# Optimization experiments

Measured on AMD Instinct MI355X. Metric: run time of the kernel, lower is better.

## Reference

```python
import jax, jax.numpy as jnp
import numpy as np

B = 2048
REAL_NL = 500
NL = 504            # ceil(500/8)*8
NZ = 50
NC = 21
GH = 512            # gru hidden
LRF = 336           # low_res_features
CHS = [336, 168, 84, 42]  # deconv channel ladder
EPS = 1e-5


def setup_inputs() -> dict:
    key = jax.random.key(0)
    ks = iter(jax.random.split(key, 40))
    d = {}
    d["X"] = jax.random.normal(next(ks), (B, REAL_NL, NC), dtype=jnp.float32)
    d["z"] = jax.random.normal(next(ks), (B, NZ), dtype=jnp.float32)
    d["is_training"] = 0
    # Upsampler dense: Linear(NZ -> NL//8 * LRF)
    d["dense_W"] = jax.random.normal(next(ks), (NL // 8 * LRF, NZ), dtype=jnp.float32) * 0.05
    d["dense_b"] = jnp.zeros((NL // 8 * LRF,), dtype=jnp.float32)
    for i in range(3):
        cin, cout = CHS[i], CHS[i + 1]
        d[f"dc{i}_W"] = jax.random.normal(next(ks), (cin, cout, 2), dtype=jnp.float32) * 0.05
        d[f"bn{i}_g"] = jnp.ones((cout,), dtype=jnp.float32)
        d[f"bn{i}_b"] = jnp.zeros((cout,), dtype=jnp.float32)
        d[f"bn{i}_m"] = jax.random.normal(next(ks), (cout,), dtype=jnp.float32) * 0.1
        d[f"bn{i}_v"] = jax.random.uniform(next(ks), (cout,), dtype=jnp.float32, minval=0.5, maxval=1.5)
        d[f"prelu{i}"] = jnp.full((1,), 0.25, dtype=jnp.float32)
    # project_x: Conv1d(NC->NC, k=1) == linear
    d["w_px"] = jax.random.normal(next(ks), (NC, NC), dtype=jnp.float32) * 0.05
    d["b_px"] = jnp.zeros((NC,), dtype=jnp.float32)
    # GRU (1 layer): input = 42 + NC = 63
    gin = CHS[3] + NC
    d["w_ih"] = jax.random.normal(next(ks), (3 * GH, gin), dtype=jnp.float32) * 0.05
    d["w_hh"] = jax.random.normal(next(ks), (3 * GH, GH), dtype=jnp.float32) * 0.05
    d["b_ih"] = jnp.zeros((3 * GH,), dtype=jnp.float32)
    d["b_hh"] = jnp.zeros((3 * GH,), dtype=jnp.float32)
    # output_x: Conv1d(GH->NC, k=1)
    d["w_out"] = jax.random.normal(next(ks), (NC, GH), dtype=jnp.float32) * 0.05
    d["b_out"] = jnp.zeros((NC,), dtype=jnp.float32)
    return d


def _upsample(z, dense_W, dense_b, dcs, bns, alphas):
    b = z.shape[0]
    h = (z @ dense_W.T + dense_b).reshape(b, LRF, NL // 8)  # [B, 336, 63]
    for i in range(3):
        W = dcs[i]  # [cin, cout, 2]
        t = h.shape[-1]
        # ConvTranspose1d k=2 s=2: out[..., 2t+k] = sum_c in[...,c,t] * W[c,:,k]
        h = jnp.einsum('bct,cok->botk', h, W).reshape(b, W.shape[1], 2 * t)
        g, bb, m, v = bns[i]
        h = (h - m[:, None]) * (g[:, None] / jnp.sqrt(v[:, None] + EPS)) + bb[:, None]
        a = alphas[i]
        h = jnp.where(h >= 0, h, a[0] * h)
    return h  # [B, 42, NL]


def reference(X, z, is_training,
              dense_W, dense_b,
              dc0_W, bn0_g, bn0_b, bn0_m, bn0_v, prelu0,
              dc1_W, bn1_g, bn1_b, bn1_m, bn1_v, prelu1,
              dc2_W, bn2_g, bn2_b, bn2_m, bn2_v, prelu2,
              w_px, b_px, w_ih, w_hh, b_ih, b_hh, w_out, b_out):
    h = _upsample(z, dense_W, dense_b,
                  [dc0_W, dc1_W, dc2_W],
                  [(bn0_g, bn0_b, bn0_m, bn0_v), (bn1_g, bn1_b, bn1_m, bn1_v), (bn2_g, bn2_b, bn2_m, bn2_v)],
                  [prelu0, prelu1, prelu2])
    b = z.shape[0]
    hseq = jnp.transpose(h, (2, 0, 1))  # [NL, B, 42]

    def step(carry, h_t):
        gru_h, x1h = carry                       # [B,GH], [B,NC]
        px = x1h @ w_px.T + b_px                 # project_x (1x1 conv)
        x_in = jnp.concatenate([h_t, px], axis=-1)  # [B, 63]
        gi = x_in @ w_ih.T + b_ih
        gh = gru_h @ w_hh.T + b_hh
        ir, iz, inn = jnp.split(gi, 3, axis=-1)
        hr, hz, hn = jnp.split(gh, 3, axis=-1)
        r = jax.nn.sigmoid(ir + hr)
        zt = jax.nn.sigmoid(iz + hz)
        n = jnp.tanh(inn + r * hn)
        h_new = (1.0 - zt) * n + zt * gru_h
        logit = h_new @ w_out.T + b_out          # [B, NC]
        x1h_new = jax.nn.one_hot(jnp.argmax(logit, axis=-1), NC, dtype=logit.dtype)
        return (h_new, x1h_new), logit

    init = (jnp.zeros((b, GH), dtype=z.dtype), jnp.zeros((b, NC), dtype=z.dtype))
    _, logits = jax.lax.scan(step, init, hseq)   # [NL, B, NC]
    out = jnp.transpose(logits, (1, 0, 2))[:, :REAL_NL, :]
    return out
```

## Files before the change

kernel.cpp:

```cpp
#include <hip/hip_runtime.h>
#include <math.h>

#define NLFULL 504
#define REAL_NL 500
#define BATCH 2048
#define NZ 50
#define NC 21
#define GHID 512
#define EPSB 1e-5f

typedef __attribute__((ext_vector_type(4))) float f32x4;
typedef __attribute__((ext_vector_type(8))) short short8;

__device__ __forceinline__ unsigned short f2bf(float x) {
    unsigned u = __builtin_bit_cast(unsigned, x);
    unsigned r = (u + 0x7FFFu + ((u >> 16) & 1u)) >> 16;
    return (unsigned short)r;
}
__device__ __forceinline__ float bf2f(unsigned short h) {
    unsigned u = ((unsigned)h) << 16;
    return __builtin_bit_cast(float, u);
}

__global__ __launch_bounds__(512) void upsample_kernel(
    const float* __restrict__ z, const float* __restrict__ dW, const float* __restrict__ db,
    const float* __restrict__ W0, const float* __restrict__ g0, const float* __restrict__ bb0,
    const float* __restrict__ m0, const float* __restrict__ v0, const float* __restrict__ al0,
    const float* __restrict__ W1, const float* __restrict__ g1, const float* __restrict__ bb1,
    const float* __restrict__ m1, const float* __restrict__ v1, const float* __restrict__ al1,
    const float* __restrict__ W2, const float* __restrict__ g2, const float* __restrict__ bb2,
    const float* __restrict__ m2, const float* __restrict__ v2, const float* __restrict__ al2,
    float* __restrict__ hseq)
{
    __shared__ float bufA[5712];
    __shared__ float bufB[5544];
    __shared__ float zl[52];

    const int b   = blockIdx.x;
    const int ta  = blockIdx.y * 16;
    const int nt0 = min(16, 63 - ta);
    const int tid = threadIdx.x;

    if (tid < NZ) zl[tid] = z[b * NZ + tid];
    __syncthreads();

    for (int i = tid; i < 336 * nt0; i += 512) {
        int c = i % 336, tt = i / 336;
        int row = c * 63 + ta + tt;
        const float* wr = dW + (size_t)row * NZ;
        float s = db[row];
        #pragma unroll
        for (int n = 0; n < NZ; ++n) s += zl[n] * wr[n];
        bufA[c * 17 + tt] = s;
    }
    __syncthreads();

    const float a0 = al0[0], a1 = al1[0], a2 = al2[0];

    for (int i = tid; i < 168 * 2 * nt0; i += 512) {
        int o = i % 168, tt1 = i / 168;
        int tt = tt1 >> 1, k = tt1 & 1;
        const float* wp = W0 + o * 2 + k;
        float s = 0.f;
        for (int c = 0; c < 336; ++c) s += bufA[c * 17 + tt] * wp[c * 336];
        float sc = g0[o] / sqrtf(v0[o] + EPSB);
        s = (s - m0[o]) * sc + bb0[o];
        s = (s >= 0.f) ? s : a0 * s;
        bufB[o * 33 + tt1] = s;
    }
    __syncthreads();

    for (int i = tid; i < 84 * 4 * nt0; i += 512) {
        int o = i % 84, tt2 = i / 84;
        int tt1 = tt2 >> 1, k = tt2 & 1;
        const float* wp = W1 + o * 2 + k;
        float s = 0.f;
        for (int c = 0; c < 168; ++c) s += bufB[c * 33 + tt1] * wp[c * 168];
        float sc = g1[o] / sqrtf(v1[o] + EPSB);
        s = (s - m1[o]) * sc + bb1[o];
        s = (s >= 0.f) ? s : a1 * s;
        bufA[o * 65 + tt2] = s;
    }
    __syncthreads();

    for (int i = tid; i < 42 * 8 * nt0; i += 512) {
        int o = i % 42, tt3 = i / 42;
        int tt2 = tt3 >> 1, k = tt3 & 1;
        const float* wp = W2 + o * 2 + k;
        float s = 0.f;
        for (int c = 0; c < 84; ++c) s += bufA[c * 65 + tt2] * wp[c * 84];
        float sc = g2[o] / sqrtf(v2[o] + EPSB);
        s = (s - m2[o]) * sc + bb2[o];
        s = (s >= 0.f) ? s : a2 * s;
        int t3 = 8 * ta + tt3;
        hseq[(size_t)t3 * (BATCH * 42) + b * 42 + o] = s;
    }
}

__global__ void table_kernel(const float* __restrict__ w_px, const float* __restrict__ b_px,
                             const float* __restrict__ w_ih, const float* __restrict__ b_ih,
                             float* __restrict__ table)
{
    int i = blockIdx.x * 256 + threadIdx.x;
    if (i >= 22 * 1536) return;
    int e = i / 1536, jg = i % 1536;
    const float* wih = w_ih + jg * 63 + 42;
    float s = b_ih[jg];
    #pragma unroll
    for (int jp = 0; jp < NC; ++jp) {
        float px = b_px[jp] + (e < NC ? w_px[jp * NC + e] : 0.f);
        s += px * wih[jp];
    }
    table[i] = s;
}

__global__ void pack_whh_kernel(const float* __restrict__ w_hh,
                                unsigned short* __restrict__ pH,
                                unsigned short* __restrict__ pM,
                                unsigned short* __restrict__ pL)
{
    int i = blockIdx.x * 256 + threadIdx.x;
    if (i >= 3 * 32 * 16 * 512) return;
    int e = i & 7, l = (i >> 3) & 63, kf = (i >> 9) & 15, nf = (i >> 13) & 31, g = i >> 18;
    int n = nf * 16 + (l & 15);
    int k = kf * 32 + ((l >> 4) << 3) + e;
    float v = w_hh[(size_t)(g * GHID + n) * GHID + k];
    unsigned short h1 = f2bf(v);       float r1 = v - bf2f(h1);
    unsigned short h2 = f2bf(r1);      float r2 = r1 - bf2f(h2);
    unsigned short h3 = f2bf(r2);
    pH[i] = h1; pM[i] = h2; pL[i] = h3;
}

__global__ void pack_wih_kernel(const float* __restrict__ w_ih,
                                unsigned short* __restrict__ pH,
                                unsigned short* __restrict__ pM,
                                unsigned short* __restrict__ pL)
{
    int i = blockIdx.x * 256 + threadIdx.x;
    if (i >= 3 * 32 * 2 * 512) return;
    int e = i & 7, l = (i >> 3) & 63, kf = (i >> 9) & 1, nf = (i >> 10) & 31, g = i >> 15;
    int n = nf * 16 + (l & 15);
    int k = kf * 32 + ((l >> 4) << 3) + e;
    float v = (k < 42) ? w_ih[(size_t)(g * GHID + n) * 63 + k] : 0.f;
    unsigned short h1 = f2bf(v);       float r1 = v - bf2f(h1);
    unsigned short h2 = f2bf(r1);      float r2 = r1 - bf2f(h2);
    unsigned short h3 = f2bf(r2);
    pH[i] = h1; pM[i] = h2; pL[i] = h3;
}

__global__ void init_kernel(unsigned short* __restrict__ hH, unsigned short* __restrict__ hM,
                            unsigned short* __restrict__ hL, int* __restrict__ idx)
{
    int i = blockIdx.x * 256 + threadIdx.x;
    if (i < BATCH * GHID) { hH[i] = 0; hM[i] = 0; hL[i] = 0; }
    if (i < BATCH) idx[i] = NC;
}

#define MFMA6(acc, aH_, aM_, aL_, bH_, bM_, bL_)                                  \
    acc = __builtin_amdgcn_mfma_f32_16x16x32_bf16(aH_, bH_, acc, 0, 0, 0);        \
    acc = __builtin_amdgcn_mfma_f32_16x16x32_bf16(aH_, bM_, acc, 0, 0, 0);        \
    acc = __builtin_amdgcn_mfma_f32_16x16x32_bf16(aM_, bH_, acc, 0, 0, 0);        \
    acc = __builtin_amdgcn_mfma_f32_16x16x32_bf16(aH_, bL_, acc, 0, 0, 0);        \
    acc = __builtin_amdgcn_mfma_f32_16x16x32_bf16(aL_, bH_, acc, 0, 0, 0);        \
    acc = __builtin_amdgcn_mfma_f32_16x16x32_bf16(aM_, bM_, acc, 0, 0, 0);

__global__ __launch_bounds__(128) void gru_gates_mfma(
    const unsigned short* __restrict__ hpH, const unsigned short* __restrict__ hpM,
    const unsigned short* __restrict__ hpL,
    const float* __restrict__ ht,
    const int* __restrict__ idx, const float* __restrict__ table,
    const unsigned short* __restrict__ whhH, const unsigned short* __restrict__ whhM,
    const unsigned short* __restrict__ whhL,
    const unsigned short* __restrict__ wihH, const unsigned short* __restrict__ wihM,
    const unsigned short* __restrict__ wihL,
    const float* __restrict__ b_hh,
    unsigned short* __restrict__ hnH, unsigned short* __restrict__ hnM,
    unsigned short* __restrict__ hnL)
{
    const int l  = threadIdx.x & 63;
    const int wv = threadIdx.x >> 6;
    const int m0 = blockIdx.x * 64 + wv * 32;
    const int nf0 = blockIdx.y * 2;
    const int lrow = l & 15;
    const int lk = (l >> 4) << 3;

    f32x4 accRZ[2][2][2];
    f32x4 accIN[2][2];
    f32x4 accHN[2][2];
    #pragma unroll
    for (int a = 0; a < 2; ++a)
        #pragma unroll
        for (int b = 0; b < 2; ++b) {
            accRZ[0][a][b] = (f32x4)0.f; accRZ[1][a][b] = (f32x4)0.f;
            accIN[a][b] = (f32x4)0.f;    accHN[a][b] = (f32x4)0.f;
        }

    const size_t arow0 = (size_t)(m0 + lrow) * GHID + lk;
    const size_t arow1 = arow0 + 16 * GHID;

    for (int kf = 0; kf < 16; ++kf) {
        short8 aH[2], aM[2], aL[2];
        aH[0] = *(const short8*)(hpH + arow0 + kf * 32);
        aM[0] = *(const short8*)(hpM + arow0 + kf * 32);
        aL[0] = *(const short8*)(hpL + arow0 + kf * 32);
        aH[1] = *(const short8*)(hpH + arow1 + kf * 32);
        aM[1] = *(const short8*)(hpM + arow1 + kf * 32);
        aL[1] = *(const short8*)(hpL + arow1 + kf * 32);
        #pragma unroll
        for (int g = 0; g < 3; ++g) {
            #pragma unroll
            for (int ni = 0; ni < 2; ++ni) {
                size_t boff = ((size_t)((g * 32 + nf0 + ni) * 16 + kf) << 9) + (l << 3);
                short8 bH = *(const short8*)(whhH + boff);
                short8 bM = *(const short8*)(whhM + boff);
                short8 bL = *(const short8*)(whhL + boff);
                #pragma unroll
                for (int mi = 0; mi < 2; ++mi) {
                    f32x4* acc = (g == 2) ? &accHN[mi][ni] : &accRZ[g][mi][ni];
                    MFMA6((*acc), aH[mi], aM[mi], aL[mi], bH, bM, bL);
                }
            }
        }
    }

    #pragma unroll
    for (int kf = 0; kf < 2; ++kf) {
        short8 aH[2], aM[2], aL[2];
        #pragma unroll
        for (int mi = 0; mi < 2; ++mi) {
            const float* rp = ht + (size_t)(m0 + mi * 16 + lrow) * 42;
            #pragma unroll
            for (int e = 0; e < 8; ++e) {
                int k = kf * 32 + lk + e;
                float f = (k < 42) ? rp[k] : 0.f;
                unsigned short h1 = f2bf(f);  float r1 = f - bf2f(h1);
                unsigned short h2 = f2bf(r1); float r2 = r1 - bf2f(h2);
                aH[mi][e] = (short)h1;
                aM[mi][e] = (short)h2;
                aL[mi][e] = (short)f2bf(r2);
            }
        }
        #pragma unroll
        for (int g = 0; g < 3; ++g) {
            #pragma unroll
            for (int ni = 0; ni < 2; ++ni) {
                size_t boff = ((size_t)((g * 32 + nf0 + ni) * 2 + kf) << 9) + (l << 3);
                short8 bH = *(const short8*)(wihH + boff);
                short8 bM = *(const short8*)(wihM + boff);
                short8 bL = *(const short8*)(wihL + boff);
                #pragma unroll
                for (int mi = 0; mi < 2; ++mi) {
                    f32x4* acc = (g == 2) ? &accIN[mi][ni] : &accRZ[g][mi][ni];
                    MFMA6((*acc), aH[mi], aM[mi], aL[mi], bH, bM, bL);
                }
            }
        }
    }

    #pragma unroll
    for (int ni = 0; ni < 2; ++ni) {
        int c = (nf0 + ni) * 16 + lrow;
        float bhr = b_hh[c], bhz = b_hh[GHID + c], bhn = b_hh[2 * GHID + c];
        #pragma unroll
        for (int mi = 0; mi < 2; ++mi) {
            #pragma unroll
            for (int r = 0; r < 4; ++r) {
                int m = m0 + mi * 16 + ((l >> 4) << 2) + r;
                const float* tb = table + idx[m] * 1536;
                float rv = accRZ[0][mi][ni][r] + bhr + tb[c];
                float zv = accRZ[1][mi][ni][r] + bhz + tb[GHID + c];
                float rg = 1.f / (1.f + expf(-rv));
                float zg = 1.f / (1.f + expf(-zv));
                float nv = accIN[mi][ni][r] + tb[2 * GHID + c] + rg * (accHN[mi][ni][r] + bhn);
                float ng = tanhf(nv);
                size_t off = (size_t)m * GHID + c;
                float hpv = bf2f(hpH[off]) + bf2f(hpM[off]) + bf2f(hpL[off]);
                float hnv = (1.f - zg) * ng + zg * hpv;
                unsigned short h1 = f2bf(hnv);  float r1 = hnv - bf2f(h1);
                unsigned short h2 = f2bf(r1);   float r2 = r1 - bf2f(h2);
                hnH[off] = h1;
                hnM[off] = h2;
                hnL[off] = f2bf(r2);
            }
        }
    }
}

__global__ __launch_bounds__(256) void gru_logits(
    const unsigned short* __restrict__ hH, const unsigned short* __restrict__ hM,
    const unsigned short* __restrict__ hL,
    const float* __restrict__ w_out, const float* __restrict__ b_out,
    float* __restrict__ out, int* __restrict__ idx, int t)
{
    const int wave = threadIdx.x >> 6, lane = threadIdx.x & 63;
    const int b = blockIdx.x * 4 + wave;

    const size_t base = (size_t)b * GHID + lane * 8;
    float hv[8];
    #pragma unroll
    for (int j = 0; j < 8; ++j)
        hv[j] = bf2f(hH[base + j]) + bf2f(hM[base + j]) + bf2f(hL[base + j]);

    float acc[NC];
    #pragma unroll
    for (int c = 0; c < NC; ++c) {
        const float* wr = w_out + c * GHID + lane * 8;
        float s = 0.f;
        #pragma unroll
        for (int j = 0; j < 8; ++j) s += hv[j] * wr[j];
        acc[c] = s;
    }
    #pragma unroll
    for (int off = 32; off > 0; off >>= 1) {
        #pragma unroll
        for (int c = 0; c < NC; ++c) acc[c] += __shfl_xor(acc[c], off);
    }
    float best = -1e30f; int bi = 0;
    #pragma unroll
    for (int c = 0; c < NC; ++c) {
        acc[c] += b_out[c];
        if (acc[c] > best) { best = acc[c]; bi = c; }
    }
    if (t < REAL_NL && lane < NC)
        out[(size_t)b * (REAL_NL * NC) + t * NC + lane] = acc[lane];
    if (lane == 0) idx[b] = bi;
}

extern "C" void kernel_launch(void* const* d_in, const int* in_sizes, int n_in,
                              void* d_out, int out_size, void* d_ws, size_t ws_size,
                              hipStream_t stream)
{
    const float* z    = (const float*)d_in[1];
    const float* dW   = (const float*)d_in[3];
    const float* db   = (const float*)d_in[4];
    const float* W0   = (const float*)d_in[5];
    const float* g0   = (const float*)d_in[6];
    const float* bb0  = (const float*)d_in[7];
    const float* m0   = (const float*)d_in[8];
    const float* v0   = (const float*)d_in[9];
    const float* al0  = (const float*)d_in[10];
    const float* W1   = (const float*)d_in[11];
    const float* g1   = (const float*)d_in[12];
    const float* bb1  = (const float*)d_in[13];
    const float* m1   = (const float*)d_in[14];
    const float* v1   = (const float*)d_in[15];
    const float* al1  = (const float*)d_in[16];
    const float* W2   = (const float*)d_in[17];
    const float* g2   = (const float*)d_in[18];
    const float* bb2  = (const float*)d_in[19];
    const float* m2   = (const float*)d_in[20];
    const float* v2   = (const float*)d_in[21];
    const float* al2  = (const float*)d_in[22];
    const float* w_px = (const float*)d_in[23];
    const float* b_px = (const float*)d_in[24];
    const float* w_ih = (const float*)d_in[25];
    const float* w_hh = (const float*)d_in[26];
    const float* b_ih = (const float*)d_in[27];
    const float* b_hh = (const float*)d_in[28];
    const float* w_out= (const float*)d_in[29];
    const float* b_out= (const float*)d_in[30];
    float* out = (float*)d_out;

    float* ws = (float*)d_ws;
    float* hseq = ws;
    unsigned short* hAH = (unsigned short*)(hseq + (size_t)NLFULL * BATCH * 42);
    unsigned short* hAM = hAH + (size_t)BATCH * GHID;
    unsigned short* hAL = hAM + (size_t)BATCH * GHID;
    unsigned short* hBH = hAL + (size_t)BATCH * GHID;
    unsigned short* hBM = hBH + (size_t)BATCH * GHID;
    unsigned short* hBL = hBM + (size_t)BATCH * GHID;
    unsigned short* whhH = hBL + (size_t)BATCH * GHID;
    unsigned short* whhM = whhH + 3 * 32 * 16 * 512;
    unsigned short* whhL = whhM + 3 * 32 * 16 * 512;
    unsigned short* wihH = whhL + 3 * 32 * 16 * 512;
    unsigned short* wihM = wihH + 3 * 32 * 2 * 512;
    unsigned short* wihL = wihM + 3 * 32 * 2 * 512;
    float* table = (float*)(wihL + 3 * 32 * 2 * 512);
    int*   idx   = (int*)(table + 22 * 1536);

    upsample_kernel<<<dim3(BATCH, 4), 512, 0, stream>>>(
        z, dW, db,
        W0, g0, bb0, m0, v0, al0,
        W1, g1, bb1, m1, v1, al1,
        W2, g2, bb2, m2, v2, al2,
        hseq);

    table_kernel<<<(22 * 1536 + 255) / 256, 256, 0, stream>>>(w_px, b_px, w_ih, b_ih, table);
    pack_whh_kernel<<<(3 * 32 * 16 * 512 + 255) / 256, 256, 0, stream>>>(w_hh, whhH, whhM, whhL);
    pack_wih_kernel<<<(3 * 32 * 2 * 512 + 255) / 256, 256, 0, stream>>>(w_ih, wihH, wihM, wihL);
    init_kernel<<<(BATCH * GHID + 255) / 256, 256, 0, stream>>>(hAH, hAM, hAL, idx);

    for (int t = 0; t < NLFULL; ++t) {
        const unsigned short* pH = (t & 1) ? hBH : hAH;
        const unsigned short* pM = (t & 1) ? hBM : hAM;
        const unsigned short* pL = (t & 1) ? hBL : hAL;
        unsigned short* nH = (t & 1) ? hAH : hBH;
        unsigned short* nM = (t & 1) ? hAM : hBM;
        unsigned short* nL = (t & 1) ? hAL : hBL;
        gru_gates_mfma<<<dim3(32, 16), 128, 0, stream>>>(
            pH, pM, pL, hseq + (size_t)t * BATCH * 42, idx, table,
            whhH, whhM, whhL, wihH, wihM, wihL, b_hh, nH, nM, nL);
        gru_logits<<<512, 256, 0, stream>>>(nH, nM, nL, w_out, b_out, out, idx, t);
    }
}
```

Measured before the change: 38.53 ms.

## Switch GRU split-precision from bf16x3 to scaled fp16x2 with new tiling

Replaces the three-way bf16 split of hidden state and weights with a two-way fp16 split (hi plus a 2048-scaled low residual), cutting the MFMAs per product from six to three and lowering memory traffic for the hidden state and weights. The low-order cross terms go into separate accumulators that are rescaled in the epilogue. The gates kernel now runs 4 waves per block in a 2x2 M/N arrangement with a transposed grid. The logits kernel is rewritten to stage w_out in shared memory, with four threads per row. fp16 has a narrower range, so accuracy depends on values staying in range, and the logits launch now has only 32 blocks.

```diff
diff --git a/kernel.cpp b/kernel.cpp
--- a/kernel.cpp
+++ b/kernel.cpp
@@ -8,18 +8,15 @@
 #define NC 21
 #define GHID 512
 #define EPSB 1e-5f
+#define LO_SCALE 2048.0f
+#define INV_LO (1.0f / 2048.0f)
 
 typedef __attribute__((ext_vector_type(4))) float f32x4;
-typedef __attribute__((ext_vector_type(8))) short short8;
-
-__device__ __forceinline__ unsigned short f2bf(float x) {
-    unsigned u = __builtin_bit_cast(unsigned, x);
-    unsigned r = (u + 0x7FFFu + ((u >> 16) & 1u)) >> 16;
-    return (unsigned short)r;
-}
-__device__ __forceinline__ float bf2f(unsigned short h) {
-    unsigned u = ((unsigned)h) << 16;
-    return __builtin_bit_cast(float, u);
+typedef __attribute__((ext_vector_type(8))) _Float16 half8;
+
+__device__ __forceinline__ void split2(float x, _Float16& hi, _Float16& lo) {
+    hi = (_Float16)x;
+    lo = (_Float16)((x - (float)hi) * LO_SCALE);
 }
 
 __global__ __launch_bounds__(512) void upsample_kernel(
@@ -115,9 +112,7 @@
 }
 
 __global__ void pack_whh_kernel(const float* __restrict__ w_hh,
-                                unsigned short* __restrict__ pH,
-                                unsigned short* __restrict__ pM,
-                                unsigned short* __restrict__ pL)
+                                _Float16* __restrict__ pH, _Float16* __restrict__ pL)
 {
     int i = blockIdx.x * 256 + threadIdx.x;
     if (i >= 3 * 32 * 16 * 512) return;
@@ -125,16 +120,12 @@
     int n = nf * 16 + (l & 15);
     int k = kf * 32 + ((l >> 4) << 3) + e;
     float v = w_hh[(size_t)(g * GHID + n) * GHID + k];
-    unsigned short h1 = f2bf(v);       float r1 = v - bf2f(h1);
-    unsigned short h2 = f2bf(r1);      float r2 = r1 - bf2f(h2);
-    unsigned short h3 = f2bf(r2);
-    pH[i] = h1; pM[i] = h2; pL[i] = h3;
+    _Float16 hi, lo; split2(v, hi, lo);
+    pH[i] = hi; pL[i] = lo;
 }
 
 __global__ void pack_wih_kernel(const float* __restrict__ w_ih,
-                                unsigned short* __restrict__ pH,
-                                unsigned short* __restrict__ pM,
-                                unsigned short* __restrict__ pL)
+                                _Float16* __restrict__ pH, _Float16* __restrict__ pL)
 {
     int i = blockIdx.x * 256 + threadIdx.x;
     if (i >= 3 * 32 * 2 * 512) return;
@@ -142,82 +133,75 @@
     int n = nf * 16 + (l & 15);
     int k = kf * 32 + ((l >> 4) << 3) + e;
     float v = (k < 42) ? w_ih[(size_t)(g * GHID + n) * 63 + k] : 0.f;
-    unsigned short h1 = f2bf(v);       float r1 = v - bf2f(h1);
-    unsigned short h2 = f2bf(r1);      float r2 = r1 - bf2f(h2);
-    unsigned short h3 = f2bf(r2);
-    pH[i] = h1; pM[i] = h2; pL[i] = h3;
-}
-
-__global__ void init_kernel(unsigned short* __restrict__ hH, unsigned short* __restrict__ hM,
-                            unsigned short* __restrict__ hL, int* __restrict__ idx)
+    _Float16 hi, lo; split2(v, hi, lo);
+    pH[i] = hi; pL[i] = lo;
+}
+
+__global__ void init_kernel(_Float16* __restrict__ hH, _Float16* __restrict__ hL,
+                            int* __restrict__ idx)
 {
     int i = blockIdx.x * 256 + threadIdx.x;
-    if (i < BATCH * GHID) { hH[i] = 0; hM[i] = 0; hL[i] = 0; }
+    if (i < BATCH * GHID) { hH[i] = (_Float16)0.f; hL[i] = (_Float16)0.f; }
     if (i < BATCH) idx[i] = NC;
 }
 
-#define MFMA6(acc, aH_, aM_, aL_, bH_, bM_, bL_)                                  \
-    acc = __builtin_amdgcn_mfma_f32_16x16x32_bf16(aH_, bH_, acc, 0, 0, 0);        \
-    acc = __builtin_amdgcn_mfma_f32_16x16x32_bf16(aH_, bM_, acc, 0, 0, 0);        \
-    acc = __builtin_amdgcn_mfma_f32_16x16x32_bf16(aM_, bH_, acc, 0, 0, 0);        \
-    acc = __builtin_amdgcn_mfma_f32_16x16x32_bf16(aH_, bL_, acc, 0, 0, 0);        \
-    acc = __builtin_amdgcn_mfma_f32_16x16x32_bf16(aL_, bH_, acc, 0, 0, 0);        \
-    acc = __builtin_amdgcn_mfma_f32_16x16x32_bf16(aM_, bM_, acc, 0, 0, 0);
-
-__global__ __launch_bounds__(128) void gru_gates_mfma(
-    const unsigned short* __restrict__ hpH, const unsigned short* __restrict__ hpM,
-    const unsigned short* __restrict__ hpL,
+#define MFMA3(mainA, crossA, aH_, aL_, bH_, bL_)                                   \
+    mainA  = __builtin_amdgcn_mfma_f32_16x16x32_f16(aH_, bH_, mainA, 0, 0, 0);     \
+    crossA = __builtin_amdgcn_mfma_f32_16x16x32_f16(aH_, bL_, crossA, 0, 0, 0);    \
+    crossA = __builtin_amdgcn_mfma_f32_16x16x32_f16(aL_, bH_, crossA, 0, 0, 0);
+
+__global__ __launch_bounds__(256) void gru_gates_mfma(
+    const _Float16* __restrict__ hpH, const _Float16* __restrict__ hpL,
     const float* __restrict__ ht,
     const int* __restrict__ idx, const float* __restrict__ table,
-    const unsigned short* __restrict__ whhH, const unsigned short* __restrict__ whhM,
-    const unsigned short* __restrict__ whhL,
-    const unsigned short* __restrict__ wihH, const unsigned short* __restrict__ wihM,
-    const unsigned short* __restrict__ wihL,
+    const _Float16* __restrict__ whhH, const _Float16* __restrict__ whhL,
+    const _Float16* __restrict__ wihH, const _Float16* __restrict__ wihL,
     const float* __restrict__ b_hh,
-    unsigned short* __restrict__ hnH, unsigned short* __restrict__ hnM,
-    unsigned short* __restrict__ hnL)
-{
-    const int l  = threadIdx.x & 63;
-    const int wv = threadIdx.x >> 6;
-    const int m0 = blockIdx.x * 64 + wv * 32;
-    const int nf0 = blockIdx.y * 2;
+    _Float16* __restrict__ hnH, _Float16* __restrict__ hnL)
+{
+    const int l   = threadIdx.x & 63;
+    const int wv  = threadIdx.x >> 6;
+    const int wM  = wv >> 1, wN = wv & 1;
+    const int m0  = blockIdx.y * 64 + wM * 32;
+    const int nfB = blockIdx.x * 4 + wN * 2;
     const int lrow = l & 15;
     const int lk = (l >> 4) << 3;
 
-    f32x4 accRZ[2][2][2];
-    f32x4 accIN[2][2];
-    f32x4 accHN[2][2];
+    f32x4 aRZ[2][2][2], xRZ[2][2][2];
+    f32x4 aIN[2][2], xIN[2][2];
+    f32x4 aHN[2][2], xHN[2][2];
     #pragma unroll
     for (int a = 0; a < 2; ++a)
         #pragma unroll
         for (int b = 0; b < 2; ++b) {
-            accRZ[0][a][b] = (f32x4)0.f; accRZ[1][a][b] = (f32x4)0.f;
-            accIN[a][b] = (f32x4)0.f;    accHN[a][b] = (f32x4)0.f;
+            aRZ[0][a][b] = (f32x4)0.f; aRZ[1][a][b] = (f32x4)0.f;
+            xRZ[0][a][b] = (f32x4)0.f; xRZ[1][a][b] = (f32x4)0.f;
+            aIN[a][b] = (f32x4)0.f; xIN[a][b] = (f32x4)0.f;
+            aHN[a][b] = (f32x4)0.f; xHN[a][b] = (f32x4)0.f;
         }
 
     const size_t arow0 = (size_t)(m0 + lrow) * GHID + lk;
     const size_t arow1 = arow0 + 16 * GHID;
 
+    #pragma unroll 2
     for (int kf = 0; kf < 16; ++kf) {
-        short8 aH[2], aM[2], aL[2];
-        aH[0] = *(const short8*)(hpH + arow0 + kf * 32);
-        aM[0] = *(const short8*)(hpM + arow0 + kf * 32);
-        aL[0] = *(const short8*)(hpL + arow0 + kf * 32);
-        aH[1] = *(const short8*)(hpH + arow1 + kf * 32);
-        aM[1] = *(const short8*)(hpM + arow1 + kf * 32);
-        aL[1] = *(const short8*)(hpL + arow1 + kf * 32);
+        half8 aH[2], aL[2];
+        aH[0] = *(const half8*)(hpH + arow0 + kf * 32);
+        aL[0] = *(const half8*)(hpL + arow0 + kf * 32);
+        aH[1] = *(const half8*)(hpH + arow1 + kf * 32);
+        aL[1] = *(const half8*)(hpL + arow1 + kf * 32);
         #pragma unroll
         for (int g = 0; g < 3; ++g) {
             #pragma unroll
             for (int ni = 0; ni < 2; ++ni) {
-                size_t boff = ((size_t)((g * 32 + nf0 + ni) * 16 + kf) << 9) + (l << 3);
-                short8 bH = *(const short8*)(whhH + boff);
-                short8 bM = *(const short8*)(whhM + boff);
-                short8 bL = *(const short8*)(whhL + boff);
+                size_t boff = ((size_t)((g * 32 + nfB + ni) * 16 + kf) << 9) + (l << 3);
+                half8 bH = *(const half8*)(whhH + boff);
+                half8 bL = *(const half8*)(whhL + boff);
                 #pragma unroll
                 for (int mi = 0; mi < 2; ++mi) {
-                    f32x4* acc = (g == 2) ? &accHN[mi][ni] : &accRZ[g][mi][ni];
-                    MFMA6((*acc), aH[mi], aM[mi], aL[mi], bH, bM, bL);
+                    f32x4* am = (g == 2) ? &aHN[mi][ni] : &aRZ[g][mi][ni];
+                    f32x4* xm = (g == 2) ? &xHN[mi][ni] : &xRZ[g][mi][ni];
+                    MFMA3((*am), (*xm), aH[mi], aL[mi], bH, bL);
                 }
             }
         }
@@ -225,7 +209,7 @@
 
     #pragma unroll
     for (int kf = 0; kf < 2; ++kf) {
-        short8 aH[2], aM[2], aL[2];
+        half8 aH[2], aL[2];
         #pragma unroll
         for (int mi = 0; mi < 2; ++mi) {
             const float* rp = ht + (size_t)(m0 + mi * 16 + lrow) * 42;
@@ -233,25 +217,22 @@
             for (int e = 0; e < 8; ++e) {
                 int k = kf * 32 + lk + e;
                 float f = (k < 42) ? rp[k] : 0.f;
-                unsigned short h1 = f2bf(f);  float r1 = f - bf2f(h1);
-                unsigned short h2 = f2bf(r1); float r2 = r1 - bf2f(h2);
-                aH[mi][e] = (short)h1;
-                aM[mi][e] = (short)h2;
-                aL[mi][e] = (short)f2bf(r2);
+                _Float16 hi, lo; split2(f, hi, lo);
+                aH[mi][e] = hi; aL[mi][e] = lo;
             }
         }
         #pragma unroll
         for (int g = 0; g < 3; ++g) {
             #pragma unroll
             for (int ni = 0; ni < 2; ++ni) {
-                size_t boff = ((size_t)((g * 32 + nf0 + ni) * 2 + kf) << 9) + (l << 3);
-                short8 bH = *(const short8*)(wihH + boff);
-                short8 bM = *(const short8*)(wihM + boff);
-                short8 bL = *(const short8*)(wihL + boff);
+                size_t boff = ((size_t)((g * 32 + nfB + ni) * 2 + kf) << 9) + (l << 3);
+                half8 bH = *(const half8*)(wihH + boff);
+                half8 bL = *(const half8*)(wihL + boff);
                 #pragma unroll
                 for (int mi = 0; mi < 2; ++mi) {
-                    f32x4* acc = (g == 2) ? &accIN[mi][ni] : &accRZ[g][mi][ni];
-                    MFMA6((*acc), aH[mi], aM[mi], aL[mi], bH, bM, bL);
+                    f32x4* am = (g == 2) ? &aIN[mi][ni] : &aRZ[g][mi][ni];
+                    f32x4* xm = (g == 2) ? &xIN[mi][ni] : &xRZ[g][mi][ni];
+                    MFMA3((*am), (*xm), aH[mi], aL[mi], bH, bL);
                 }
             }
         }
@@ -259,7 +240,7 @@
 
     #pragma unroll
     for (int ni = 0; ni < 2; ++ni) {
-        int c = (nf0 + ni) * 16 + lrow;
+        int c = (nfB + ni) * 16 + lrow;
         float bhr = b_hh[c], bhz = b_hh[GHID + c], bhn = b_hh[2 * GHID + c];
         #pragma unroll
         for (int mi = 0; mi < 2; ++mi) {
@@ -267,63 +248,67 @@
             for (int r = 0; r < 4; ++r) {
                 int m = m0 + mi * 16 + ((l >> 4) << 2) + r;
                 const float* tb = table + idx[m] * 1536;
-                float rv = accRZ[0][mi][ni][r] + bhr + tb[c];
-                float zv = accRZ[1][mi][ni][r] + bhz + tb[GHID + c];
+                float rv = aRZ[0][mi][ni][r] + xRZ[0][mi][ni][r] * INV_LO + bhr + tb[c];
+                float zv = aRZ[1][mi][ni][r] + xRZ[1][mi][ni][r] * INV_LO + bhz + tb[GHID + c];
                 float rg = 1.f / (1.f + expf(-rv));
                 float zg = 1.f / (1.f + expf(-zv));
-                float nv = accIN[mi][ni][r] + tb[2 * GHID + c] + rg * (accHN[mi][ni][r] + bhn);
-                float ng = tanhf(nv);
+                float hnp = aHN[mi][ni][r] + xHN[mi][ni][r] * INV_LO + bhn;
+                float inp = aIN[mi][ni][r] + xIN[mi][ni][r] * INV_LO + tb[2 * GHID + c];
+                float ng = tanhf(inp + rg * hnp);
                 size_t off = (size_t)m * GHID + c;
-                float hpv = bf2f(hpH[off]) + bf2f(hpM[off]) + bf2f(hpL[off]);
+                float hpv = (float)hpH[off] + (float)hpL[off] * INV_LO;
                 float hnv = (1.f - zg) * ng + zg * hpv;
-                unsigned short h1 = f2bf(hnv);  float r1 = hnv - bf2f(h1);
-                unsigned short h2 = f2bf(r1);   float r2 = r1 - bf2f(h2);
-                hnH[off] = h1;
-                hnM[off] = h2;
-                hnL[off] = f2bf(r2);
+                _Float16 hi, lo; split2(hnv, hi, lo);
+                hnH[off] = hi; hnL[off] = lo;
             }
         }
     }
 }
 
 __global__ __launch_bounds__(256) void gru_logits(
-    const unsigned short* __restrict__ hH, const unsigned short* __restrict__ hM,
-    const unsigned short* __restrict__ hL,
+    const _Float16* __restrict__ hH, const _Float16* __restrict__ hL,
     const float* __restrict__ w_out, const float* __restrict__ b_out,
     float* __restrict__ out, int* __restrict__ idx, int t)
 {
-    const int wave = threadIdx.x >> 6, lane = threadIdx.x & 63;
-    const int b = blockIdx.x * 4 + wave;
-
-    const size_t base = (size_t)b * GHID + lane * 8;
-    float hv[8];
-    #pragma unroll
-    for (int j = 0; j < 8; ++j)
-        hv[j] = bf2f(hH[base + j]) + bf2f(hM[base + j]) + bf2f(hL[base + j]);
+    __shared__ float wsm[NC * GHID];
+    const int tid = threadIdx.x;
+    for (int i = tid; i < NC * GHID; i += 256) wsm[i] = w_out[i];
+    __syncthreads();
+
+    const int r = tid >> 2, q = tid & 3;
+    const int row = blockIdx.x * 64 + r;
+    const _Float16* ph = hH + (size_t)row * GHID + q * 128;
+    const _Float16* pl = hL + (size_t)row * GHID + q * 128;
 
     float acc[NC];
     #pragma unroll
+    for (int c = 0; c < NC; ++c) acc[c] = 0.f;
+
+    for (int kk = 0; kk < 128; ++kk) {
+        float hval = (float)ph[kk] + (float)pl[kk] * INV_LO;
+        const float* wp = wsm + q * 128 + kk;
+        #pragma unroll
+        for (int c = 0; c < NC; ++c) acc[c] += hval * wp[c * GHID];
+    }
+    #pragma unroll
     for (int c = 0; c < NC; ++c) {
-        const float* wr = w_out + c * GHID + lane * 8;
-        float s = 0.f;
-        #pragma unroll
-        for (int j = 0; j < 8; ++j) s += hv[j] * wr[j];
-        acc[c] = s;
-    }
-    #pragma unroll
-    for (int off = 32; off > 0; off >>= 1) {
-        #pragma unroll
-        for (int c = 0; c < NC; ++c) acc[c] += __shfl_xor(acc[c], off);
-    }
-    float best = -1e30f; int bi = 0;
-    #pragma unroll
-    for (int c = 0; c < NC; ++c) {
-        acc[c] += b_out[c];
-        if (acc[c] > best) { best = acc[c]; bi = c; }
-    }
-    if (t < REAL_NL && lane < NC)
-        out[(size_t)b * (REAL_NL * NC) + t * NC + lane] = acc[lane];
-    if (lane == 0) idx[b] = bi;
+        acc[c] += __shfl_xor(acc[c], 1);
+        acc[c] += __shfl_xor(acc[c], 2);
+    }
+    if (q == 0) {
+        float best = -1e30f; int bi = 0;
+        #pragma unroll
+        for (int c = 0; c < NC; ++c) {
+            acc[c] += b_out[c];
+            if (acc[c] > best) { best = acc[c]; bi = c; }
+        }
+        if (t < REAL_NL) {
+            float* op = out + (size_t)row * (REAL_NL * NC) + (size_t)t * NC;
+            #pragma unroll
+            for (int c = 0; c < NC; ++c) op[c] = acc[c];
+        }
+        idx[row] = bi;
+    }
 }
 
 extern "C" void kernel_launch(void* const* d_in, const int* in_sizes, int n_in,
@@ -363,18 +348,14 @@
 
     float* ws = (float*)d_ws;
     float* hseq = ws;
-    unsigned short* hAH = (unsigned short*)(hseq + (size_t)NLFULL * BATCH * 42);
-    unsigned short* hAM = hAH + (size_t)BATCH * GHID;
-    unsigned short* hAL = hAM + (size_t)BATCH * GHID;
-    unsigned short* hBH = hAL + (size_t)BATCH * GHID;
-    unsigned short* hBM = hBH + (size_t)BATCH * GHID;
-    unsigned short* hBL = hBM + (size_t)BATCH * GHID;
-    unsigned short* whhH = hBL + (size_t)BATCH * GHID;
-    unsigned short* whhM = whhH + 3 * 32 * 16 * 512;
-    unsigned short* whhL = whhM + 3 * 32 * 16 * 512;
-    unsigned short* wihH = whhL + 3 * 32 * 16 * 512;
-    unsigned short* wihM = wihH + 3 * 32 * 2 * 512;
-    unsigned short* wihL = wihM + 3 * 32 * 2 * 512;
+    _Float16* hAH = (_Float16*)(hseq + (size_t)NLFULL * BATCH * 42);
+    _Float16* hAL = hAH + (size_t)BATCH * GHID;
+    _Float16* hBH = hAL + (size_t)BATCH * GHID;
+    _Float16* hBL = hBH + (size_t)BATCH * GHID;
+    _Float16* whhH = hBL + (size_t)BATCH * GHID;
+    _Float16* whhL = whhH + 3 * 32 * 16 * 512;
+    _Float16* wihH = whhL + 3 * 32 * 16 * 512;
+    _Float16* wihL = wihH + 3 * 32 * 2 * 512;
     float* table = (float*)(wihL + 3 * 32 * 2 * 512);
     int*   idx   = (int*)(table + 22 * 1536);
 
@@ -386,20 +367,18 @@
         hseq);
 
     table_kernel<<<(22 * 1536 + 255) / 256, 256, 0, stream>>>(w_px, b_px, w_ih, b_ih, table);
-    pack_whh_kernel<<<(3 * 32 * 16 * 512 + 255) / 256, 256, 0, stream>>>(w_hh, whhH, whhM, whhL);
-    pack_wih_kernel<<<(3 * 32 * 2 * 512 + 255) / 256, 256, 0, stream>>>(w_ih, wihH, wihM, wihL);
-    init_kernel<<<(BATCH * GHID + 255) / 256, 256, 0, stream>>>(hAH, hAM, hAL, idx);
+    pack_whh_kernel<<<(3 * 32 * 16 * 512 + 255) / 256, 256, 0, stream>>>(w_hh, whhH, whhL);
+    pack_wih_kernel<<<(3 * 32 * 2 * 512 + 255) / 256, 256, 0, stream>>>(w_ih, wihH, wihL);
+    init_kernel<<<(BATCH * GHID + 255) / 256, 256, 0, stream>>>(hAH, hAL, idx);
 
     for (int t = 0; t < NLFULL; ++t) {
-        const unsigned short* pH = (t & 1) ? hBH : hAH;
-        const unsigned short* pM = (t & 1) ? hBM : hAM;
-        const unsigned short* pL = (t & 1) ? hBL : hAL;
-        unsigned short* nH = (t & 1) ? hAH : hBH;
-        unsigned short* nM = (t & 1) ? hAM : hBM;
-        unsigned short* nL = (t & 1) ? hAL : hBL;
-        gru_gates_mfma<<<dim3(32, 16), 128, 0, stream>>>(
-            pH, pM, pL, hseq + (size_t)t * BATCH * 42, idx, table,
-            whhH, whhM, whhL, wihH, wihM, wihL, b_hh, nH, nM, nL);
-        gru_logits<<<512, 256, 0, stream>>>(nH, nM, nL, w_out, b_out, out, idx, t);
-    }
-}
+        const _Float16* pH = (t & 1) ? hBH : hAH;
+        const _Float16* pL = (t & 1) ? hBL : hAL;
+        _Float16* nH = (t & 1) ? hAH : hBH;
+        _Float16* nL = (t & 1) ? hAL : hBL;
+        gru_gates_mfma<<<dim3(8, 32), 256, 0, stream>>>(
+            pH, pL, hseq + (size_t)t * BATCH * 42, idx, table,
+            whhH, whhL, wihH, wihL, b_hh, nH, nL);
+        gru_logits<<<32, 256, 0, stream>>>(nH, nL, w_out, b_out, out, idx, t);
+    }
+}
```

New measurement: 49.89 ms. 1.29x slower.
